# Optimization experiments

Measured on AMD Instinct MI355X. Metric: run time of the kernel, lower is better.

## Reference

```python
import jax, jax.numpy as jnp
import numpy as np
import math

NUM_HEADS = 16
HIDDEN = 1024
HEAD_DIM = HIDDEN // NUM_HEADS
MAX_POS = 512
BUCKET = 256
SCALE = 1.0 / math.sqrt(3.0 * HEAD_DIM)


def _make_log_bucket_position(rel_pos):
    # rel_pos: int32 [S, S]
    mid = BUCKET // 2
    rp = rel_pos.astype(jnp.float32)
    sign = jnp.sign(rp)
    abs_pos = jnp.where((rel_pos < mid) & (rel_pos > -mid), float(mid - 1), jnp.abs(rp))
    log_pos = jnp.ceil(jnp.log(abs_pos / mid) * (mid - 1) / math.log((MAX_POS - 1) / mid)) + mid
    bucket_pos = jnp.where(abs_pos <= mid, rp, log_pos * sign)
    return bucket_pos.astype(jnp.int32)


def _get_rel_pos(num_positions):
    ids = jnp.arange(num_positions, dtype=jnp.int32)
    rel_pos = ids[:, None] - ids[None, :]  # [S, S]
    return _make_log_bucket_position(rel_pos)


def setup_inputs() -> dict:
    key = jax.random.key(0)
    ks = jax.random.split(key, 10)
    B, S = 8, 512
    s_in = 1.0 / math.sqrt(HIDDEN)
    inputs = jax.random.normal(ks[0], (B, S, HIDDEN), dtype=jnp.float32)
    rel_embeddings = jax.random.normal(ks[1], (B, 2 * BUCKET, HIDDEN), dtype=jnp.float32)
    Wq = jax.random.normal(ks[2], (HIDDEN, NUM_HEADS, HEAD_DIM), dtype=jnp.float32) * s_in
    Wk = jax.random.normal(ks[3], (HIDDEN, NUM_HEADS, HEAD_DIM), dtype=jnp.float32) * s_in
    Wv = jax.random.normal(ks[4], (HIDDEN, NUM_HEADS, HEAD_DIM), dtype=jnp.float32) * s_in
    bq = jnp.zeros((NUM_HEADS, HEAD_DIM), dtype=jnp.float32)
    bk = jnp.zeros((NUM_HEADS, HEAD_DIM), dtype=jnp.float32)
    bv = jnp.zeros((NUM_HEADS, HEAD_DIM), dtype=jnp.float32)
    Wo = jax.random.normal(ks[5], (HIDDEN, HIDDEN), dtype=jnp.float32) * s_in
    bo = jnp.zeros((HIDDEN,), dtype=jnp.float32)
    return {"inputs": inputs, "rel_embeddings": rel_embeddings,
            "Wq": Wq, "bq": bq, "Wk": Wk, "bk": bk, "Wv": Wv, "bv": bv,
            "Wo": Wo, "bo": bo}


def reference(inputs, rel_embeddings, Wq, bq, Wk, bk, Wv, bv, Wo, bo):
    B, S, _ = inputs.shape
    # projections: [B,S,H,D]
    query = jnp.einsum('bsc,chd->bshd', inputs, Wq) + bq
    key = jnp.einsum('bsc,chd->bshd', inputs, Wk) + bk
    value = jnp.einsum('bsc,chd->bshd', inputs, Wv) + bv

    # content-content scores: [B,H,S_q,S_k]
    scores = jnp.einsum('bkhd,bqhd->bhqk', key, query) * SCALE

    # relative position projections on rel_embeddings [B,P,hidden], P=2*BUCKET
    pos_query = jnp.einsum('bpc,chd->bphd', rel_embeddings, Wq) + bq
    pos_key = jnp.einsum('bpc,chd->bphd', rel_embeddings, Wk) + bk

    rel_pos = _get_rel_pos(S)  # [S,S] int32
    span = BUCKET

    # c2p: query vs pos_key -> [B,H,S,P], gather along last axis
    c2p = jnp.einsum('bphd,bqhd->bhqp', pos_key, query)
    c2p_pos = jnp.clip(rel_pos + span, 0, 2 * span - 1)  # [S,S]
    c2p_idx = jnp.broadcast_to(c2p_pos[None, None], (B, NUM_HEADS, S, S))
    c2p = jnp.take_along_axis(c2p, c2p_idx, axis=3) * SCALE

    # p2c: key vs pos_query -> [B,H,S,P], gather then transpose
    p2c = jnp.einsum('bphd,bkhd->bhkp', pos_query, key)
    p2c_pos = jnp.clip(-rel_pos + span, 0, 2 * span - 1)
    p2c_idx = jnp.broadcast_to(p2c_pos[None, None], (B, NUM_HEADS, S, S))
    p2c = jnp.take_along_axis(p2c, p2c_idx, axis=3)
    p2c = jnp.swapaxes(p2c, 2, 3) * SCALE

    scores = scores + c2p + p2c
    probs = jax.nn.softmax(scores.astype(jnp.float32), axis=-1).astype(inputs.dtype)

    # attend: [B,S,H,D] -> [B,S,hidden]
    attn_out = jnp.einsum('bhqk,bkhd->bqhd', probs, value)
    attn_out = attn_out.reshape(B, S, HIDDEN)
    return jnp.einsum('bsc,cd->bsd', attn_out, Wo) + bo
```

## Files before the change

### kernel.cpp

```cpp
#include <hip/hip_runtime.h>

#define NUM_HEADS 16
#define HEAD_DIM  64
#define HIDDEN    1024
#define SEQ       512
#define BATCH     8
#define NBH       128
#define POSN      512
#define SCALE_F   0.07216878364870323f

typedef __attribute__((ext_vector_type(8))) short  short8;
typedef __attribute__((ext_vector_type(4))) short  short4_t;
typedef __attribute__((ext_vector_type(4))) float  floatx4;

#define GLDS16(gsrc, ldst) \
    __builtin_amdgcn_global_load_lds((const __attribute__((address_space(1))) void*)(gsrc), \
                                     (__attribute__((address_space(3))) void*)(ldst), 16, 0, 0)

__device__ __forceinline__ float bits2f(short s) {
    union { unsigned u; float f; } x;
    x.u = ((unsigned)(unsigned short)s) << 16;
    return x.f;
}
__device__ __forceinline__ short f2bits(float f) {
    union { float f; unsigned u; } x;
    x.f = f;
    unsigned r = x.u + 0x7fffu + ((x.u >> 16) & 1u);
    return (short)(r >> 16);
}

__global__ __launch_bounds__(256)
void prep_all(const float* __restrict__ a, const float* __restrict__ b,
              short* __restrict__ oa, short* __restrict__ ob,
              const float* __restrict__ w0, const float* __restrict__ w1,
              const float* __restrict__ w2, const float* __restrict__ w3,
              short* __restrict__ o0, short* __restrict__ o1,
              short* __restrict__ o2, short* __restrict__ o3,
              int* __restrict__ ftab)
{
    __shared__ float tile[64][65];
    const int bid = blockIdx.x, t = threadIdx.x;

    if (bid < 4096) {
        const int idx = bid * 256 + t;
        floatx4 va = ((const floatx4*)a)[idx];
        floatx4 vb = ((const floatx4*)b)[idx];
        short4_t ra, rb;
#pragma unroll
        for (int i = 0; i < 4; i++) { ra[i] = f2bits(va[i]); rb[i] = f2bits(vb[i]); }
        ((short4_t*)oa)[idx] = ra;
        ((short4_t*)ob)[idx] = rb;
        return;
    }
    if (bid < 5120) {
        const int r = bid - 4096;
        const int z = r >> 8, rem = r & 255;
        const float* src = (z == 0) ? w0 : (z == 1) ? w1 : (z == 2) ? w2 : w3;
        short*       dst = (z == 0) ? o0 : (z == 1) ? o1 : (z == 2) ? o2 : o3;
        const int c0 = (rem & 15) * 64, n0 = (rem >> 4) * 64;
#pragma unroll
        for (int j = 0; j < 16; j++) {
            const int e = t + j * 256;
            tile[e >> 6][e & 63] = src[(long)(c0 + (e >> 6)) * 1024 + n0 + (e & 63)];
        }
        __syncthreads();
#pragma unroll
        for (int j = 0; j < 16; j++) {
            const int e = t + j * 256;
            dst[(long)(n0 + (e >> 6)) * 1024 + c0 + (e & 63)] = f2bits(tile[e & 63][e >> 6]);
        }
        return;
    }
    const int i = (bid - 5120) * 256 + t;
    if (i >= 1023) return;
    const int delta = i - 511;
    const float Cf = (float)log(511.0 / 128.0);
    float absp = (delta < 128 && delta > -128) ? 127.0f : fabsf((float)delta);
    float bucket;
    if (absp <= 128.0f) {
        bucket = (float)delta;
    } else {
        float lp = ceilf((logf(absp * (1.0f / 128.0f)) * 127.0f) / Cf) + 128.0f;
        bucket = (delta > 0) ? lp : -lp;
    }
    int bi = (int)bucket + 256;
    bi = min(max(bi, 0), 511);
    ftab[i] = bi;
}

template<int MODE>
__global__ __launch_bounds__(256)
void gemm_nt(const short* __restrict__ A, long aBatch, int lda,
             const short* __restrict__ BT, long bBatch, int ldb,
             void* __restrict__ O0, void* __restrict__ O1, void* __restrict__ O2,
             long oBatch, int ldo,
             const float* __restrict__ b0, const float* __restrict__ b1,
             const float* __restrict__ b2, int Kd,
             const short* __restrict__ A2,
             void* __restrict__ O3, void* __restrict__ O4)
{
    __shared__ __align__(16) short LB[24576];

    int m0, n0, yy = 0;
    bool z1 = false;
    const int z = blockIdx.z;
    if (MODE == 6) {
        const int lin = blockIdx.x + (blockIdx.y << 5);
        const int swz = (lin & 7) * 160 + (lin >> 3);
        m0 = (swz & 31) * 128;
        yy = swz >> 5;
        z1 = (yy >= 24);
        n0 = (z1 ? (yy - 24) : yy) * 128;
    } else {
        m0 = blockIdx.x * 128;
        n0 = blockIdx.y * 128;
    }

    const short* Ab;
    const short* Bb;
    if (MODE == 6) {
        Ab = z1 ? A2 : A;
        Bb = BT;
    } else {
        Ab = A + (long)z * aBatch;
        Bb = BT + (long)z * bBatch;
    }

    const int t = threadIdx.x;
    const int l = t & 63, w = t >> 6;
    const int wm = w >> 1, wn = w & 1;
    const int lr = l & 15, lg = l >> 4;

    const int c0c = t, c1c = t + 256;
    const int r0 = c0c >> 2, cc0 = (c0c & 3) ^ ((r0 >> 1) & 3);
    const int r1 = c1c >> 2, cc1 = (c1c & 3) ^ ((r1 >> 1) & 3);

    floatx4 acc[4][4];
#pragma unroll
    for (int i = 0; i < 4; i++)
#pragma unroll
        for (int j = 0; j < 4; j++) acc[i][j] = (floatx4){0.f, 0.f, 0.f, 0.f};

    const int niter = Kd >> 5;

    {
        GLDS16(Ab + (long)(m0 + r0) * lda + cc0 * 8, LB + c0c * 8);
        GLDS16(Ab + (long)(m0 + r1) * lda + cc1 * 8, LB + c1c * 8);
        GLDS16(Bb + (long)(n0 + r0) * ldb + cc0 * 8, LB + 12288 + c0c * 8);
        GLDS16(Bb + (long)(n0 + r1) * ldb + cc1 * 8, LB + 12288 + c1c * 8);
        GLDS16(Ab + (long)(m0 + r0) * lda + 32 + cc0 * 8, LB + 4096 + c0c * 8);
        GLDS16(Ab + (long)(m0 + r1) * lda + 32 + cc1 * 8, LB + 4096 + c1c * 8);
        GLDS16(Bb + (long)(n0 + r0) * ldb + 32 + cc0 * 8, LB + 12288 + 4096 + c0c * 8);
        GLDS16(Bb + (long)(n0 + r1) * ldb + 32 + cc1 * 8, LB + 12288 + 4096 + c1c * 8);
    }

    int cbase = 0;
    int ibase = 8192;
    for (int i = 0; i < niter; i++) {
        __builtin_amdgcn_sched_barrier(0);
        if (i + 1 < niter) { asm volatile("s_waitcnt vmcnt(4)" ::: "memory"); }
        else               { asm volatile("s_waitcnt vmcnt(0)" ::: "memory"); }
        __builtin_amdgcn_s_barrier();
        __builtin_amdgcn_sched_barrier(0);
        if (i + 2 < niter) {
            const int kn = (i + 2) << 5;
            GLDS16(Ab + (long)(m0 + r0) * lda + kn + cc0 * 8, LB + ibase + c0c * 8);
            GLDS16(Ab + (long)(m0 + r1) * lda + kn + cc1 * 8, LB + ibase + c1c * 8);
            GLDS16(Bb + (long)(n0 + r0) * ldb + kn + cc0 * 8, LB + 12288 + ibase + c0c * 8);
            GLDS16(Bb + (long)(n0 + r1) * ldb + kn + cc1 * 8, LB + 12288 + ibase + c1c * 8);
        }
        const short* Asb = LB + cbase;
        const short* Bsb = LB + 12288 + cbase;
        short8 af[4], bfr[4];
#pragma unroll
        for (int i4 = 0; i4 < 4; i4++) {
            const int mr = wm * 64 + i4 * 16 + lr;
            af[i4] = *(const short8*)((const char*)Asb + mr * 64 + ((lg ^ ((mr >> 1) & 3)) * 16));
            const int nr = wn * 64 + i4 * 16 + lr;
            bfr[i4] = *(const short8*)((const char*)Bsb + nr * 64 + ((lg ^ ((nr >> 1) & 3)) * 16));
        }
#pragma unroll
        for (int i4 = 0; i4 < 4; i4++)
#pragma unroll
            for (int j4 = 0; j4 < 4; j4++)
                acc[i4][j4] = __builtin_amdgcn_mfma_f32_16x16x32_bf16(af[i4], bfr[j4], acc[i4][j4], 0, 0, 0);
        cbase += 4096; if (cbase == 12288) cbase = 0;
        ibase += 4096; if (ibase == 12288) ibase = 0;
    }
    __syncthreads();

    if (MODE == 6 && !z1 && yy >= 16) {
        short* tp = &LB[0];
#pragma unroll
        for (int i = 0; i < 4; i++)
#pragma unroll
            for (int j = 0; j < 4; j++)
#pragma unroll
                for (int e = 0; e < 4; e++) {
                    const int ml  = wm * 64 + i * 16 + lg * 4 + e;
                    const int ngl = wn * 64 + j * 16 + lr;
                    const float v = acc[i][j][e] + b2[(n0 & 1023) + ngl];
                    tp[ngl * 128 + (ml ^ ((ngl & 7) << 4))] = f2bits(v);
                }
        __syncthreads();
        const int b = m0 >> 9, s0 = m0 & 511;
        const int hb = (n0 & 1023) >> 6;
        short* dst = (short*)O2;
#pragma unroll
        for (int j = 0; j < 8; j++) {
            const int task = t + j * 256;
            const int r = task >> 4, c = task & 15;
            short8 v8 = *(const short8*)(tp + r * 128 + ((c * 8) ^ ((r & 7) << 4)));
            const int h = hb + (r >> 6), d = r & 63;
            *(short8*)(dst + ((long)((b * NUM_HEADS + h) * HEAD_DIM + d)) * SEQ + s0 + c * 8) = v8;
        }
        return;
    }

#pragma unroll
    for (int i = 0; i < 4; i++) {
#pragma unroll
        for (int j = 0; j < 4; j++) {
#pragma unroll
            for (int e = 0; e < 4; e++) {
                const int mg = m0 + wm * 64 + i * 16 + lg * 4 + e;
                const int ng = n0 + wn * 64 + j * 16 + lr;
                float v = acc[i][j][e];
                if (MODE == 1) {
                    ((short*)O0)[(long)z * oBatch + (long)mg * ldo + ng] = f2bits(v);
                } else if (MODE == 2) {
                    ((float*)O0)[(long)mg * ldo + ng] = v + b0[ng];
                } else if (MODE == 6) {
                    const int hh = ng & 1023, mat = ng >> 10;
                    const int h = hh >> 6, d = hh & 63;
                    const int b = mg >> 9, s = mg & 511;
                    v += (mat == 0 ? b0 : b1)[hh];
                    short* dst;
                    if (z1) dst = (short*)(mat == 0 ? O3 : O4);
                    else    dst = (short*)(mat == 0 ? O0 : O1);
                    dst[((long)(b * NUM_HEADS + h) * SEQ + s) * HEAD_DIM + d] = f2bits(v);
                }
            }
        }
    }
}

__global__ __launch_bounds__(512, 2)
void p2c_fused(const short* __restrict__ posQ, const short* __restrict__ K,
               const short* __restrict__ c2pf, const int* __restrict__ ftab,
               short* __restrict__ Bias)
{
    __shared__ __align__(16) short As[512 * 64];
    __shared__ __align__(16) short Bs[64 * 64];
    __shared__ short ft[1024];
    const int ko = blockIdx.x, bh = blockIdx.y;
    const int k0 = ko * 64;
    const int t = threadIdx.x, l = t & 63, w = t >> 6;
    const int lr = l & 15, lg = l >> 4;
    const short* Ab = posQ + (long)bh * SEQ * HEAD_DIM;
    const short* Kb = K + (long)bh * SEQ * HEAD_DIM;
    const short* c2pb = c2pf + (long)bh * SEQ * POSN;

    for (int i = t; i < 1024; i += 512) ft[i] = (short)((i < 1023) ? ftab[i] : 0);

#pragma unroll
    for (int j = 0; j < 8; j++) {
        const int c = j * 512 + t;
        const int row = c >> 3, pc = c & 7;
        const int cc = pc ^ (row & 7);
        GLDS16(Ab + (long)row * HEAD_DIM + cc * 8, As + c * 8);
    }
    {
        const int c = t;
        const int row = c >> 3, pc = c & 7;
        const int cc = pc ^ (row & 7);
        GLDS16(Kb + (long)(k0 + row) * HEAD_DIM + cc * 8, Bs + c * 8);
    }
    __syncthreads();

    floatx4 acc[4][4];
#pragma unroll
    for (int i = 0; i < 4; i++)
#pragma unroll
        for (int j = 0; j < 4; j++) acc[i][j] = (floatx4){0.f, 0.f, 0.f, 0.f};
#pragma unroll
    for (int ks = 0; ks < 2; ks++) {
        short8 af[4], bfr[4];
#pragma unroll
        for (int i = 0; i < 4; i++) {
            const int mr = w * 64 + i * 16 + lr;
            af[i] = *(const short8*)((char*)As + mr * 128 + (((ks * 4 + lg) ^ (mr & 7)) * 16));
            const int nr = i * 16 + lr;
            bfr[i] = *(const short8*)((char*)Bs + nr * 128 + (((ks * 4 + lg) ^ (nr & 7)) * 16));
        }
#pragma unroll
        for (int i = 0; i < 4; i++)
#pragma unroll
            for (int j = 0; j < 4; j++)
                acc[i][j] = __builtin_amdgcn_mfma_f32_16x16x32_bf16(af[i], bfr[j], acc[i][j], 0, 0, 0);
    }
    __syncthreads();

#pragma unroll
    for (int i = 0; i < 4; i++)
#pragma unroll
        for (int j = 0; j < 4; j++)
#pragma unroll
            for (int e = 0; e < 4; e++) {
                const int p = w * 64 + i * 16 + lg * 4 + e;
                const int kk = j * 16 + lr;
                As[p * 64 + (kk ^ (lg << 4))] = f2bits(acc[i][j][e]);
            }
    __syncthreads();

    short* Bb = Bias + (long)bh * SEQ * SEQ;
#pragma unroll
    for (int j = 0; j < 8; j++) {
        const int task = j * 512 + t;
        const int qt = task >> 8;
        const int kl = (task >> 2) & 63;
        const int rc = task & 3;
        const int k  = k0 + kl;
        short8 v;
#pragma unroll
        for (int i = 0; i < 8; i++) {
            const int q  = qt * 32 + rc * 8 + i;
            const int fk = (int)ft[q - k + 511];
            const float sv = bits2f(As[fk * 64 + (kl ^ (((fk >> 2) & 3) << 4))]);
            const float cv = bits2f(c2pb[(long)q * POSN + fk]);
            v[i] = f2bits(sv + cv);
        }
        *(short8*)(Bb + (((long)qt * 512 + k) << 5) + rc * 8) = v;
    }
}

__global__ __launch_bounds__(256, 4)
void attn_fused(const short* __restrict__ Q, const short* __restrict__ K,
                const short* __restrict__ Vt, const short* __restrict__ Bias,
                short* __restrict__ attnO)
{
    __shared__ __align__(16) short PS[32 * 512];
    __shared__ float red[4][32];

    const int lin  = blockIdx.x;
    const int lin2 = (lin & 7) * 256 + (lin >> 3);
    const int bh = lin2 >> 4, qt = lin2 & 15;
    const int q0 = qt * 32;
    const int t = threadIdx.x, l = t & 63, w = t >> 6;
    const int lr = l & 15, lg = l >> 4;
    const long pbase = (long)bh * SEQ * HEAD_DIM;
    const short* Qb  = Q  + pbase;
    const short* Kb  = K  + pbase;
    const short* Vtb = Vt + pbase;
    const short* Bb  = Bias + ((long)bh * 16 + qt) * (512 * 32);

    short4_t bfrag[2][8];
#pragma unroll
    for (int mt = 0; mt < 2; mt++)
#pragma unroll
        for (int nt = 0; nt < 8; nt++) {
            const int k = w * 128 + nt * 16 + lr;
            bfrag[mt][nt] = *(const short4_t*)(Bb + (long)k * 32 + mt * 16 + lg * 4);
        }

    short8 aq[2][2];
#pragma unroll
    for (int mt = 0; mt < 2; mt++)
#pragma unroll
        for (int ks = 0; ks < 2; ks++)
            aq[mt][ks] = *(const short8*)(Qb + (q0 + mt * 16 + lr) * 64 + ks * 32 + lg * 8);

    floatx4 acc[2][8];
#pragma unroll
    for (int mt = 0; mt < 2; mt++)
#pragma unroll
        for (int nt = 0; nt < 8; nt++) acc[mt][nt] = (floatx4){0.f, 0.f, 0.f, 0.f};

#pragma unroll
    for (int nt = 0; nt < 8; nt++) {
        const int kr = w * 128 + nt * 16 + lr;
        short8 kb0 = *(const short8*)(Kb + kr * 64 + lg * 8);
        short8 kb1 = *(const short8*)(Kb + kr * 64 + 32 + lg * 8);
#pragma unroll
        for (int mt = 0; mt < 2; mt++) {
            acc[mt][nt] = __builtin_amdgcn_mfma_f32_16x16x32_bf16(aq[mt][0], kb0, acc[mt][nt], 0, 0, 0);
            acc[mt][nt] = __builtin_amdgcn_mfma_f32_16x16x32_bf16(aq[mt][1], kb1, acc[mt][nt], 0, 0, 0);
        }
    }

#pragma unroll
    for (int mt = 0; mt < 2; mt++)
#pragma unroll
        for (int e = 0; e < 4; e++) {
            const int r = mt * 16 + lg * 4 + e;
            float s = 0.f;
#pragma unroll
            for (int nt = 0; nt < 8; nt++) {
                float p = __expf((acc[mt][nt][e] + bits2f(bfrag[mt][nt][e])) * SCALE_F);
                acc[mt][nt][e] = p;
                s += p;
            }
            s += __shfl_xor(s, 1); s += __shfl_xor(s, 2);
            s += __shfl_xor(s, 4); s += __shfl_xor(s, 8);
            red[w][r] = s;
#pragma unroll
            for (int nt = 0; nt < 8; nt++) {
                const int kcol = w * 128 + nt * 16 + lr;
                int byte = r * 1024 + kcol * 2;
                byte ^= (r & 7) << 4;
                *(short*)((char*)PS + byte) = f2bits(acc[mt][nt][e]);
            }
        }
    __syncthreads();

    floatx4 accO[2];
    accO[0] = (floatx4){0.f, 0.f, 0.f, 0.f};
    accO[1] = (floatx4){0.f, 0.f, 0.f, 0.f};
#pragma unroll
    for (int ks = 0; ks < 16; ks++) {
        short8 vb = *(const short8*)(Vtb + (long)(w * 16 + lr) * SEQ + ks * 32 + lg * 8);
#pragma unroll
        for (int mt = 0; mt < 2; mt++) {
            const int qr = mt * 16 + lr;
            int byte = qr * 1024 + (ks * 32 + lg * 8) * 2;
            byte ^= (qr & 7) << 4;
            short8 pa = *(const short8*)((char*)PS + byte);
            accO[mt] = __builtin_amdgcn_mfma_f32_16x16x32_bf16(pa, vb, accO[mt], 0, 0, 0);
        }
    }

    const int b = bh >> 4, h = bh & 15;
#pragma unroll
    for (int mt = 0; mt < 2; mt++)
#pragma unroll
        for (int e = 0; e < 4; e++) {
            const int r = mt * 16 + lg * 4 + e;
            const float rs = red[0][r] + red[1][r] + red[2][r] + red[3][r];
            const float v = accO[mt][e] / rs;
            attnO[((long)(b * SEQ + q0 + r)) * HIDDEN + h * HEAD_DIM + w * 16 + lr] = f2bits(v);
        }
}

extern "C" void kernel_launch(void* const* d_in, const int* in_sizes, int n_in,
                              void* d_out, int out_size, void* d_ws, size_t ws_size,
                              hipStream_t stream)
{
    const float* inputs = (const float*)d_in[0];
    const float* rel    = (const float*)d_in[1];
    const float* Wq     = (const float*)d_in[2];
    const float* bq     = (const float*)d_in[3];
    const float* Wk     = (const float*)d_in[4];
    const float* bk     = (const float*)d_in[5];
    const float* Wv     = (const float*)d_in[6];
    const float* bv     = (const float*)d_in[7];
    const float* Wo     = (const float*)d_in[8];
    const float* bo     = (const float*)d_in[9];
    float* out = (float*)d_out;

    char* ws = (char*)d_ws;
    size_t off = 0;
    auto alloc = [&](size_t bytes) -> char* {
        char* p = ws + off;
        off += (bytes + 255) & ~(size_t)255;
        return p;
    };
    short* inA   = (short*)alloc(4194304ull * 2);
    short* inRel = (short*)alloc(4194304ull * 2);
    short* WqT   = (short*)alloc(1048576ull * 2);
    short* WkT   = (short*)alloc(1048576ull * 2);
    short* WvT   = (short*)alloc(1048576ull * 2);
    short* WoT   = (short*)alloc(1048576ull * 2);
    short* Qw    = (short*)alloc(4194304ull * 2);
    short* Kw    = (short*)alloc(4194304ull * 2);
    short* Vtw   = (short*)alloc(4194304ull * 2);
    short* posQw = (short*)alloc(4194304ull * 2);
    short* posKw = (short*)alloc(4194304ull * 2);
    short* c2pW  = (short*)alloc(33554432ull * 2);
    short* BW    = (short*)alloc(33554432ull * 2);
    short* attnW = (short*)alloc(4194304ull * 2);
    int*   ftabW = (int*)alloc(4096);

    prep_all<<<5124, 256, 0, stream>>>(inputs, rel, inA, inRel,
                                       Wq, Wk, Wv, Wo, WqT, WkT, WvT, WoT, ftabW);

    gemm_nt<6><<<dim3(32, 40), 256, 0, stream>>>(inA, 0, 1024, WqT, 0, 1024,
                                                 Qw, Kw, Vtw, 0, 0, bq, bk, bv, 1024,
                                                 inRel, posQw, posKw);

    gemm_nt<1><<<dim3(4, 4, 128), 256, 0, stream>>>(Qw, 32768, 64, posKw, 32768, 64,
                                                    c2pW, nullptr, nullptr, 262144, 512,
                                                    nullptr, nullptr, nullptr, 64,
                                                    nullptr, nullptr, nullptr);

    p2c_fused<<<dim3(8, 128), 512, 0, stream>>>(posQw, Kw, c2pW, ftabW, BW);

    attn_fused<<<2048, 256, 0, stream>>>(Qw, Kw, Vtw, BW, attnW);

    gemm_nt<2><<<dim3(32, 8), 256, 0, stream>>>(attnW, 0, 1024, WoT, 0, 1024,
                                                out, nullptr, nullptr, 0, 1024, bo, nullptr, nullptr, 1024,
                                                nullptr, nullptr, nullptr);
}
```

Before: 194.8 us.

## Switch projection GEMM to BK=64 double-buffered pipeline; keep old kernel for others

The fused QKV/pos projection GEMM (MODE 6) now stages K-tiles of 64 in two LDS buffers with an 8-chunk XOR swizzle and a single __syncthreads per iteration, replacing the triple-buffered BK=32 pipeline that used explicit vmcnt waits. The aim is to halve the number of barriers and loop iterations for the largest GEMM. The old triple-buffered kernel is kept as gemm_nt3 for the c2p and output GEMMs. The cost is losing the fine-grained vmcnt overlap: each iteration's prefetch must finish before the barrier, which may expose load latency. LDS use also grows from 48KB to 64KB per block, which may lower occupancy.

```diff
diff --git a/kernel.cpp b/kernel.cpp
--- a/kernel.cpp
+++ b/kernel.cpp
@@ -99,7 +99,8 @@
              const short* __restrict__ A2,
              void* __restrict__ O3, void* __restrict__ O4)
 {
-    __shared__ __align__(16) short LB[24576];
+    __shared__ __align__(16) short As[2][128 * 64];
+    __shared__ __align__(16) short Bs[2][128 * 64];
 
     int m0, n0, yy = 0;
     bool z1 = false;
@@ -131,66 +132,56 @@
     const int wm = w >> 1, wn = w & 1;
     const int lr = l & 15, lg = l >> 4;
 
-    const int c0c = t, c1c = t + 256;
-    const int r0 = c0c >> 2, cc0 = (c0c & 3) ^ ((r0 >> 1) & 3);
-    const int r1 = c1c >> 2, cc1 = (c1c & 3) ^ ((r1 >> 1) & 3);
-
     floatx4 acc[4][4];
 #pragma unroll
     for (int i = 0; i < 4; i++)
 #pragma unroll
         for (int j = 0; j < 4; j++) acc[i][j] = (floatx4){0.f, 0.f, 0.f, 0.f};
 
-    const int niter = Kd >> 5;
-
-    {
-        GLDS16(Ab + (long)(m0 + r0) * lda + cc0 * 8, LB + c0c * 8);
-        GLDS16(Ab + (long)(m0 + r1) * lda + cc1 * 8, LB + c1c * 8);
-        GLDS16(Bb + (long)(n0 + r0) * ldb + cc0 * 8, LB + 12288 + c0c * 8);
-        GLDS16(Bb + (long)(n0 + r1) * ldb + cc1 * 8, LB + 12288 + c1c * 8);
-        GLDS16(Ab + (long)(m0 + r0) * lda + 32 + cc0 * 8, LB + 4096 + c0c * 8);
-        GLDS16(Ab + (long)(m0 + r1) * lda + 32 + cc1 * 8, LB + 4096 + c1c * 8);
-        GLDS16(Bb + (long)(n0 + r0) * ldb + 32 + cc0 * 8, LB + 12288 + 4096 + c0c * 8);
-        GLDS16(Bb + (long)(n0 + r1) * ldb + 32 + cc1 * 8, LB + 12288 + 4096 + c1c * 8);
-    }
-
-    int cbase = 0;
-    int ibase = 8192;
-    for (int i = 0; i < niter; i++) {
-        __builtin_amdgcn_sched_barrier(0);
-        if (i + 1 < niter) { asm volatile("s_waitcnt vmcnt(4)" ::: "memory"); }
-        else               { asm volatile("s_waitcnt vmcnt(0)" ::: "memory"); }
-        __builtin_amdgcn_s_barrier();
-        __builtin_amdgcn_sched_barrier(0);
-        if (i + 2 < niter) {
-            const int kn = (i + 2) << 5;
-            GLDS16(Ab + (long)(m0 + r0) * lda + kn + cc0 * 8, LB + ibase + c0c * 8);
-            GLDS16(Ab + (long)(m0 + r1) * lda + kn + cc1 * 8, LB + ibase + c1c * 8);
-            GLDS16(Bb + (long)(n0 + r0) * ldb + kn + cc0 * 8, LB + 12288 + ibase + c0c * 8);
-            GLDS16(Bb + (long)(n0 + r1) * ldb + kn + cc1 * 8, LB + 12288 + ibase + c1c * 8);
-        }
-        const short* Asb = LB + cbase;
-        const short* Bsb = LB + 12288 + cbase;
-        short8 af[4], bfr[4];
-#pragma unroll
-        for (int i4 = 0; i4 < 4; i4++) {
-            const int mr = wm * 64 + i4 * 16 + lr;
-            af[i4] = *(const short8*)((const char*)Asb + mr * 64 + ((lg ^ ((mr >> 1) & 3)) * 16));
-            const int nr = wn * 64 + i4 * 16 + lr;
-            bfr[i4] = *(const short8*)((const char*)Bsb + nr * 64 + ((lg ^ ((nr >> 1) & 3)) * 16));
-        }
-#pragma unroll
-        for (int i4 = 0; i4 < 4; i4++)
-#pragma unroll
-            for (int j4 = 0; j4 < 4; j4++)
-                acc[i4][j4] = __builtin_amdgcn_mfma_f32_16x16x32_bf16(af[i4], bfr[j4], acc[i4][j4], 0, 0, 0);
-        cbase += 4096; if (cbase == 12288) cbase = 0;
-        ibase += 4096; if (ibase == 12288) ibase = 0;
+#pragma unroll
+    for (int j = 0; j < 4; j++) {
+        const int c = (w * 4 + j) * 64 + l;
+        const int row = c >> 3, pc = c & 7;
+        const int cc = pc ^ (row & 7);
+        GLDS16(Ab + (long)(m0 + row) * lda + cc * 8, As[0] + c * 8);
+        GLDS16(Bb + (long)(n0 + row) * ldb + cc * 8, Bs[0] + c * 8);
     }
     __syncthreads();
 
+    int cur = 0;
+    for (int k0 = 0; k0 < Kd; k0 += 64, cur ^= 1) {
+        if (k0 + 64 < Kd) {
+            const int kn = k0 + 64;
+#pragma unroll
+            for (int j = 0; j < 4; j++) {
+                const int c = (w * 4 + j) * 64 + l;
+                const int row = c >> 3, pc = c & 7;
+                const int cc = pc ^ (row & 7);
+                GLDS16(Ab + (long)(m0 + row) * lda + kn + cc * 8, As[cur ^ 1] + c * 8);
+                GLDS16(Bb + (long)(n0 + row) * ldb + kn + cc * 8, Bs[cur ^ 1] + c * 8);
+            }
+        }
+#pragma unroll
+        for (int ks = 0; ks < 2; ks++) {
+            short8 af[4], bfr[4];
+#pragma unroll
+            for (int i = 0; i < 4; i++) {
+                const int mr = wm * 64 + i * 16 + lr;
+                af[i] = *(const short8*)((char*)As[cur] + mr * 128 + (((ks * 4 + lg) ^ (mr & 7)) * 16));
+                const int nr = wn * 64 + i * 16 + lr;
+                bfr[i] = *(const short8*)((char*)Bs[cur] + nr * 128 + (((ks * 4 + lg) ^ (nr & 7)) * 16));
+            }
+#pragma unroll
+            for (int i = 0; i < 4; i++)
+#pragma unroll
+                for (int j = 0; j < 4; j++)
+                    acc[i][j] = __builtin_amdgcn_mfma_f32_16x16x32_bf16(af[i], bfr[j], acc[i][j], 0, 0, 0);
+        }
+        __syncthreads();
+    }
+
     if (MODE == 6 && !z1 && yy >= 16) {
-        short* tp = &LB[0];
+        short* tp = &As[0][0];
 #pragma unroll
         for (int i = 0; i < 4; i++)
 #pragma unroll
@@ -239,6 +230,101 @@
                     if (z1) dst = (short*)(mat == 0 ? O3 : O4);
                     else    dst = (short*)(mat == 0 ? O0 : O1);
                     dst[((long)(b * NUM_HEADS + h) * SEQ + s) * HEAD_DIM + d] = f2bits(v);
+                }
+            }
+        }
+    }
+}
+
+template<int MODE>
+__global__ __launch_bounds__(256)
+void gemm_nt3(const short* __restrict__ A, long aBatch, int lda,
+              const short* __restrict__ BT, long bBatch, int ldb,
+              void* __restrict__ O0, long oBatch, int ldo,
+              const float* __restrict__ b0, int Kd)
+{
+    __shared__ __align__(16) short LB[24576];
+
+    const int z = blockIdx.z;
+    const int m0 = blockIdx.x * 128, n0 = blockIdx.y * 128;
+    const short* Ab = A + (long)z * aBatch;
+    const short* Bb = BT + (long)z * bBatch;
+
+    const int t = threadIdx.x;
+    const int l = t & 63, w = t >> 6;
+    const int wm = w >> 1, wn = w & 1;
+    const int lr = l & 15, lg = l >> 4;
+
+    const int c0c = t, c1c = t + 256;
+    const int r0 = c0c >> 2, cc0 = (c0c & 3) ^ ((r0 >> 1) & 3);
+    const int r1 = c1c >> 2, cc1 = (c1c & 3) ^ ((r1 >> 1) & 3);
+
+    floatx4 acc[4][4];
+#pragma unroll
+    for (int i = 0; i < 4; i++)
+#pragma unroll
+        for (int j = 0; j < 4; j++) acc[i][j] = (floatx4){0.f, 0.f, 0.f, 0.f};
+
+    const int niter = Kd >> 5;
+
+    {
+        GLDS16(Ab + (long)(m0 + r0) * lda + cc0 * 8, LB + c0c * 8);
+        GLDS16(Ab + (long)(m0 + r1) * lda + cc1 * 8, LB + c1c * 8);
+        GLDS16(Bb + (long)(n0 + r0) * ldb + cc0 * 8, LB + 12288 + c0c * 8);
+        GLDS16(Bb + (long)(n0 + r1) * ldb + cc1 * 8, LB + 12288 + c1c * 8);
+        GLDS16(Ab + (long)(m0 + r0) * lda + 32 + cc0 * 8, LB + 4096 + c0c * 8);
+        GLDS16(Ab + (long)(m0 + r1) * lda + 32 + cc1 * 8, LB + 4096 + c1c * 8);
+        GLDS16(Bb + (long)(n0 + r0) * ldb + 32 + cc0 * 8, LB + 12288 + 4096 + c0c * 8);
+        GLDS16(Bb + (long)(n0 + r1) * ldb + 32 + cc1 * 8, LB + 12288 + 4096 + c1c * 8);
+    }
+
+    int cbase = 0;
+    int ibase = 8192;
+    for (int i = 0; i < niter; i++) {
+        __builtin_amdgcn_sched_barrier(0);
+        if (i + 1 < niter) { asm volatile("s_waitcnt vmcnt(4)" ::: "memory"); }
+        else               { asm volatile("s_waitcnt vmcnt(0)" ::: "memory"); }
+        __builtin_amdgcn_s_barrier();
+        __builtin_amdgcn_sched_barrier(0);
+        if (i + 2 < niter) {
+            const int kn = (i + 2) << 5;
+            GLDS16(Ab + (long)(m0 + r0) * lda + kn + cc0 * 8, LB + ibase + c0c * 8);
+            GLDS16(Ab + (long)(m0 + r1) * lda + kn + cc1 * 8, LB + ibase + c1c * 8);
+            GLDS16(Bb + (long)(n0 + r0) * ldb + kn + cc0 * 8, LB + 12288 + ibase + c0c * 8);
+            GLDS16(Bb + (long)(n0 + r1) * ldb + kn + cc1 * 8, LB + 12288 + ibase + c1c * 8);
+        }
+        const short* Asb = LB + cbase;
+        const short* Bsb = LB + 12288 + cbase;
+        short8 af[4], bfr[4];
+#pragma unroll
+        for (int i4 = 0; i4 < 4; i4++) {
+            const int mr = wm * 64 + i4 * 16 + lr;
+            af[i4] = *(const short8*)((const char*)Asb + mr * 64 + ((lg ^ ((mr >> 1) & 3)) * 16));
+            const int nr = wn * 64 + i4 * 16 + lr;
+            bfr[i4] = *(const short8*)((const char*)Bsb + nr * 64 + ((lg ^ ((nr >> 1) & 3)) * 16));
+        }
+#pragma unroll
+        for (int i4 = 0; i4 < 4; i4++)
+#pragma unroll
+            for (int j4 = 0; j4 < 4; j4++)
+                acc[i4][j4] = __builtin_amdgcn_mfma_f32_16x16x32_bf16(af[i4], bfr[j4], acc[i4][j4], 0, 0, 0);
+        cbase += 4096; if (cbase == 12288) cbase = 0;
+        ibase += 4096; if (ibase == 12288) ibase = 0;
+    }
+
+#pragma unroll
+    for (int i = 0; i < 4; i++) {
+#pragma unroll
+        for (int j = 0; j < 4; j++) {
+#pragma unroll
+            for (int e = 0; e < 4; e++) {
+                const int mg = m0 + wm * 64 + i * 16 + lg * 4 + e;
+                const int ng = n0 + wn * 64 + j * 16 + lr;
+                float v = acc[i][j][e];
+                if (MODE == 1) {
+                    ((short*)O0)[(long)z * oBatch + (long)mg * ldo + ng] = f2bits(v);
+                } else {
+                    ((float*)O0)[(long)mg * ldo + ng] = v + b0[ng];
                 }
             }
         }
@@ -487,16 +573,13 @@
                                                  Qw, Kw, Vtw, 0, 0, bq, bk, bv, 1024,
                                                  inRel, posQw, posKw);
 
-    gemm_nt<1><<<dim3(4, 4, 128), 256, 0, stream>>>(Qw, 32768, 64, posKw, 32768, 64,
-                                                    c2pW, nullptr, nullptr, 262144, 512,
-                                                    nullptr, nullptr, nullptr, 64,
-                                                    nullptr, nullptr, nullptr);
+    gemm_nt3<1><<<dim3(4, 4, 128), 256, 0, stream>>>(Qw, 32768, 64, posKw, 32768, 64,
+                                                     c2pW, 262144, 512, nullptr, 64);
 
     p2c_fused<<<dim3(8, 128), 512, 0, stream>>>(posQw, Kw, c2pW, ftabW, BW);
 
     attn_fused<<<2048, 256, 0, stream>>>(Qw, Kw, Vtw, BW, attnW);
 
-    gemm_nt<2><<<dim3(32, 8), 256, 0, stream>>>(attnW, 0, 1024, WoT, 0, 1024,
-                                                out, nullptr, nullptr, 0, 1024, bo, nullptr, nullptr, 1024,
-                                                nullptr, nullptr, nullptr);
-}
+    gemm_nt3<2><<<dim3(32, 8), 256, 0, stream>>>(attnW, 0, 1024, WoT, 0, 1024,
+                                                 out, 0, 1024, bo, 1024);
+}
```

Result: no change. 192.9 us (-1.0%).
